# Performance work log

Measured on AMD Instinct MI355X. Metric: run time of the kernel, lower is better.

## Reference

```python
import jax, jax.numpy as jnp
import numpy as np

B, N, F, H, D = 2, 2048, 1024, 16, 64


def setup_inputs() -> dict:
    key = jax.random.key(0)
    ks = jax.random.split(key, 5)
    s = 0.02
    return {
        "x": jax.random.normal(ks[0], (B, N, F), jnp.float32),
        "w_qkv": (jax.random.normal(ks[1], (3 * H * D, F), jnp.float32) * s),
        "w_out": (jax.random.normal(ks[2], (F, H * D), jnp.float32) * s),
        "w_hp_pre": (jax.random.normal(ks[3], (H, H), jnp.float32) * (1.0 / H)),
        "b_hp_pre": jnp.zeros((H,), jnp.float32),
        "w_hp_post": (jax.random.normal(ks[4], (H, H), jnp.float32) * (1.0 / H)),
        "b_hp_post": jnp.zeros((H,), jnp.float32),
    }


def reference(x, w_qkv, w_out, w_hp_pre, b_hp_pre, w_hp_post, b_hp_post):
    b, n, f = x.shape
    # qkv projection; rearrange 'b n (h d qkv) -> qkv b h n d' (qkv innermost)
    proj = (x @ w_qkv.T).reshape(b, n, H, D, 3)
    q = jnp.transpose(proj[..., 0], (0, 2, 1, 3))  # b h n d
    k = jnp.transpose(proj[..., 1], (0, 2, 1, 3))
    v = jnp.transpose(proj[..., 2], (0, 2, 1, 3))
    kv = jnp.stack([k, v], axis=0)  # (2, b, h, n, d) -- returned cache

    scale = D ** -0.5
    dots = jnp.einsum('bhid,bhjd->bhij', q, k) * scale
    # pre talking-heads: 1x1 conv over head channel
    dots = jnp.einsum('gh,bhij->bgij', w_hp_pre, dots) + b_hp_pre[None, :, None, None]
    attn = jax.nn.softmax(dots, axis=-1)
    # post talking-heads
    attn = jnp.einsum('gh,bhij->bgij', w_hp_post, attn) + b_hp_post[None, :, None, None]
    out = jnp.einsum('bhij,bhjd->bhid', attn, v)
    out = jnp.transpose(out, (0, 2, 1, 3)).reshape(b, n, H * D)
    out = out @ w_out.T
    return out, kv
```

## Files before the change

### kernel.cpp

```cpp
#include <hip/hip_runtime.h>
#include <hip/hip_bf16.h>
#include <cstdint>
#include <cstddef>

#define B_ 2
#define N_ 2048
#define F_ 1024
#define H_ 16
#define D_ 64

typedef float f32x4 __attribute__((ext_vector_type(4)));
typedef short s16x8 __attribute__((ext_vector_type(8)));
typedef short s16x4 __attribute__((ext_vector_type(4)));

__device__ __forceinline__ unsigned short f2bf(float f) {
  union { __hip_bfloat16 h; unsigned short u; } c;
  c.h = __float2bfloat16(f);
  return c.u;
}
__device__ __forceinline__ float bf2f(unsigned short u) {
  union { __hip_bfloat16 h; unsigned short u; } c;
  c.u = u;
  return __bfloat162float(c.h);
}

__global__ __launch_bounds__(256) void cvt_bf16(const float* __restrict__ in,
                                                unsigned short* __restrict__ out,
                                                int n8) {
  const int t = blockIdx.x * 256 + threadIdx.x;
  if (t >= n8) return;
  const float4* p = (const float4*)in + (size_t)t * 2;
  float4 a = p[0], b = p[1];
  s16x8 o;
  o[0] = f2bf(a.x); o[1] = f2bf(a.y); o[2] = f2bf(a.z); o[3] = f2bf(a.w);
  o[4] = f2bf(b.x); o[5] = f2bf(b.y); o[6] = f2bf(b.z); o[7] = f2bf(b.w);
  *((s16x8*)out + t) = o;
}

__global__ __launch_bounds__(256) void cvt_wqkv_perm(const float* __restrict__ in,
                                                     unsigned short* __restrict__ out) {
  const int t = blockIdx.x * 256 + threadIdx.x;
  const int rowp = t >> 7;
  const int kk = (t & 127) * 8;
  const int c = rowp >> 10, rem = rowp & 1023;
  const int h = rem >> 6, d = rem & 63;
  const float* p = in + (size_t)(h * 192 + d * 3 + c) * 1024 + kk;
  float4 a = *(const float4*)p, b = *(const float4*)(p + 4);
  s16x8 o;
  o[0] = f2bf(a.x); o[1] = f2bf(a.y); o[2] = f2bf(a.z); o[3] = f2bf(a.w);
  o[4] = f2bf(b.x); o[5] = f2bf(b.y); o[6] = f2bf(b.z); o[7] = f2bf(b.w);
  *((s16x8*)&out[(size_t)rowp * 1024 + kk]) = o;
}

__global__ __launch_bounds__(256) void cvt_sum(const float* __restrict__ a,
                                               const float* __restrict__ b,
                                               unsigned short* __restrict__ out) {
  const int t = blockIdx.x * 256 + threadIdx.x;
  float4 x = *((const float4*)a + t);
  float4 y = *((const float4*)b + t);
  s16x4 o;
  o[0] = f2bf(x.x + y.x); o[1] = f2bf(x.y + y.y);
  o[2] = f2bf(x.z + y.z); o[3] = f2bf(x.w + y.w);
  *((s16x4*)out + t) = o;
}

template <int MODE>
__global__ __launch_bounds__(256) void gemm_bf16(const unsigned short* __restrict__ A,
                                                 const unsigned short* __restrict__ W,
                                                 float* __restrict__ o0,
                                                 unsigned short* __restrict__ oQ,
                                                 unsigned short* __restrict__ oK,
                                                 unsigned short* __restrict__ oVt) {
  __shared__ unsigned short As[128 * 72];
  __shared__ unsigned short Bs[128 * 72];
  const int m0 = blockIdx.y * 128, c0 = blockIdx.x * 128;
  const int tid = threadIdx.x;
  const int wave = tid >> 6, lane = tid & 63;
  const int wm = (wave & 1) * 64, wn = (wave >> 1) * 64;
  const int lm = lane & 15, lq = lane >> 4;
  f32x4 acc[4][4] = {};
  for (int k0 = 0; k0 < 1024; k0 += 64) {
#pragma unroll
    for (int it = 0; it < 4; ++it) {
      const int chunk = it * 256 + tid;
      const int row = chunk >> 3, kq = (chunk & 7) * 8;
      *(float4*)&As[row * 72 + kq] = *(const float4*)&A[(size_t)(m0 + row) * 1024 + k0 + kq];
      *(float4*)&Bs[row * 72 + kq] = *(const float4*)&W[(size_t)(c0 + row) * 1024 + k0 + kq];
    }
    __syncthreads();
#pragma unroll
    for (int ks = 0; ks < 2; ++ks) {
      s16x8 af[4], bfr[4];
#pragma unroll
      for (int i = 0; i < 4; ++i) {
        af[i] = *(const s16x8*)&As[(wm + i * 16 + lm) * 72 + ks * 32 + lq * 8];
        bfr[i] = *(const s16x8*)&Bs[(wn + i * 16 + lm) * 72 + ks * 32 + lq * 8];
      }
#pragma unroll
      for (int i = 0; i < 4; ++i)
#pragma unroll
        for (int j = 0; j < 4; ++j)
          acc[i][j] = __builtin_amdgcn_mfma_f32_16x16x32_bf16(af[i], bfr[j], acc[i][j], 0, 0, 0);
    }
    __syncthreads();
  }
  if (MODE == 1) {
#pragma unroll
    for (int i = 0; i < 4; ++i)
#pragma unroll
      for (int j = 0; j < 4; ++j)
#pragma unroll
        for (int r = 0; r < 4; ++r) {
          const int m = m0 + wm + i * 16 + lq * 4 + r;
          const int col = c0 + wn + j * 16 + lm;
          o0[(size_t)m * 1024 + col] = acc[i][j][r];
        }
  } else {
    const int cls = blockIdx.x >> 3;
    const int colbase = (blockIdx.x & 7) * 128;
    if (cls == 0) {
#pragma unroll
      for (int i = 0; i < 4; ++i)
#pragma unroll
        for (int j = 0; j < 4; ++j) {
          const int cl = colbase + wn + j * 16 + lm;
          const int h = cl >> 6, d = cl & 63;
#pragma unroll
          for (int r = 0; r < 4; ++r) {
            const int m = m0 + wm + i * 16 + lq * 4 + r;
            const int bb = m >> 11, n = m & 2047;
            oQ[(((size_t)bb * H_ + h) * N_ + n) * D_ + d] = f2bf(acc[i][j][r]);
          }
        }
    } else if (cls == 1) {
#pragma unroll
      for (int i = 0; i < 4; ++i)
#pragma unroll
        for (int j = 0; j < 4; ++j) {
          const int cl = colbase + wn + j * 16 + lm;
          const int h = cl >> 6, d = cl & 63;
#pragma unroll
          for (int r = 0; r < 4; ++r) {
            const int m = m0 + wm + i * 16 + lq * 4 + r;
            const int bb = m >> 11, n = m & 2047;
            const size_t idx = (((size_t)bb * H_ + h) * N_ + n) * D_ + d;
            o0[idx] = acc[i][j][r];
            oK[idx] = f2bf(acc[i][j][r]);
          }
        }
    } else {
#pragma unroll
      for (int i = 0; i < 4; ++i) {
        const int n0 = m0 + wm + i * 16 + lq * 4;
        const int bb = n0 >> 11, nl = n0 & 2047;
#pragma unroll
        for (int j = 0; j < 4; ++j) {
          const int cl = colbase + wn + j * 16 + lm;
          const int h = cl >> 6, d = cl & 63;
          s16x4 vp;
#pragma unroll
          for (int r = 0; r < 4; ++r) {
            const size_t idx = (((size_t)bb * H_ + h) * N_ + nl + r) * D_ + d;
            o0[(size_t)B_ * H_ * N_ * D_ + idx] = acc[i][j][r];
            vp[r] = (short)f2bf(acc[i][j][r]);
          }
          *(s16x4*)&oVt[(((size_t)bb * H_ + h) * D_ + d) * N_ + nl] = vp;
        }
      }
    }
  }
}

#define SS_I 648
#define SS_J 20
#define PS_G 1160
#define PS_I 36

__global__ __launch_bounds__(512) void attn_l(const unsigned short* __restrict__ Qb,
                                              const unsigned short* __restrict__ Kb,
                                              const float* __restrict__ wpre,
                                              const float* __restrict__ bpre,
                                              float* __restrict__ l_glob) {
  __shared__ unsigned short Ssh[32 * SS_I];
  const int tid = threadIdx.x;
  const int wave = tid >> 6, lane = tid & 63;
  const int lm = lane & 15, lq = lane >> 4;
  const int b = blockIdx.z, jh = blockIdx.y;
  const int i0 = blockIdx.x * 32;
  const int j00 = jh * 1024;
  const int h0 = wave * 2;

  s16x8 aq[2][2][2];
#pragma unroll
  for (int hh = 0; hh < 2; ++hh)
#pragma unroll
    for (int mi = 0; mi < 2; ++mi)
#pragma unroll
      for (int ks = 0; ks < 2; ++ks)
        aq[hh][mi][ks] = *(const s16x8*)&Qb[(((size_t)(b * H_ + h0 + hh) * N_) + i0 + mi * 16 + lm) * D_ + ks * 32 + lq * 8];

  s16x8 apre;
#pragma unroll
  for (int t = 0; t < 8; ++t) apre[t] = 0;
  if (lq < 2)
#pragma unroll
    for (int t = 0; t < 8; ++t) apre[t] = (short)f2bf(wpre[lm * 16 + lq * 8 + t] * 0.125f);
  float bpre_r[4];
#pragma unroll
  for (int r = 0; r < 4; ++r) bpre_r[r] = bpre[lq * 4 + r];

  float lacc[4][4] = {};

  for (int js = 0; js < 1024; js += 32) {
    const int j0 = j00 + js;
    s16x8 bk[2][2][2];
#pragma unroll
    for (int hh = 0; hh < 2; ++hh)
#pragma unroll
      for (int jt = 0; jt < 2; ++jt)
#pragma unroll
        for (int ks = 0; ks < 2; ++ks)
          bk[hh][jt][ks] = *(const s16x8*)&Kb[(((size_t)(b * H_ + h0 + hh) * N_) + j0 + jt * 16 + lm) * D_ + ks * 32 + lq * 8];
    f32x4 cs[2][2][2];
#pragma unroll
    for (int hh = 0; hh < 2; ++hh)
#pragma unroll
      for (int mi = 0; mi < 2; ++mi)
#pragma unroll
        for (int jt = 0; jt < 2; ++jt) {
          f32x4 c = {};
          c = __builtin_amdgcn_mfma_f32_16x16x32_bf16(aq[hh][mi][0], bk[hh][jt][0], c, 0, 0, 0);
          c = __builtin_amdgcn_mfma_f32_16x16x32_bf16(aq[hh][mi][1], bk[hh][jt][1], c, 0, 0, 0);
          cs[hh][mi][jt] = c;
        }
    __syncthreads();
#pragma unroll
    for (int hh = 0; hh < 2; ++hh)
#pragma unroll
      for (int mi = 0; mi < 2; ++mi)
#pragma unroll
        for (int jt = 0; jt < 2; ++jt)
#pragma unroll
          for (int r = 0; r < 4; ++r)
            Ssh[(mi * 16 + lq * 4 + r) * SS_I + (jt * 16 + lm) * SS_J + h0 + hh] = f2bf(cs[hh][mi][jt][r]);
    __syncthreads();
#pragma unroll
    for (int ii = 0; ii < 4; ++ii) {
      const int i_loc = wave * 4 + ii;
#pragma unroll
      for (int jt = 0; jt < 2; ++jt) {
        s16x8 bs;
#pragma unroll
        for (int t = 0; t < 8; ++t) bs[t] = 0;
        if (lq < 2) {
          s16x4 p0 = *(const s16x4*)&Ssh[i_loc * SS_I + (jt * 16 + lm) * SS_J + lq * 8];
          s16x4 p1 = *(const s16x4*)&Ssh[i_loc * SS_I + (jt * 16 + lm) * SS_J + lq * 8 + 4];
          bs[0] = p0[0]; bs[1] = p0[1]; bs[2] = p0[2]; bs[3] = p0[3];
          bs[4] = p1[0]; bs[5] = p1[1]; bs[6] = p1[2]; bs[7] = p1[3];
        }
        f32x4 c = {};
        c = __builtin_amdgcn_mfma_f32_16x16x32_bf16(apre, bs, c, 0, 0, 0);
#pragma unroll
        for (int r = 0; r < 4; ++r) lacc[ii][r] += __expf(c[r] + bpre_r[r]);
      }
    }
  }
#pragma unroll
  for (int ii = 0; ii < 4; ++ii)
#pragma unroll
    for (int r = 0; r < 4; ++r) {
      float v = lacc[ii][r];
      v += __shfl_xor(v, 1); v += __shfl_xor(v, 2);
      v += __shfl_xor(v, 4); v += __shfl_xor(v, 8);
      if (lm == 0)
        atomicAdd(&l_glob[((size_t)b * N_ + i0 + wave * 4 + ii) * H_ + lq * 4 + r], v);
    }
}

__global__ __launch_bounds__(512) void attn_av(const unsigned short* __restrict__ Qb,
                                               const unsigned short* __restrict__ Kb,
                                               const unsigned short* __restrict__ Vt,
                                               const float* __restrict__ wpre,
                                               const float* __restrict__ bpre,
                                               const float* __restrict__ wpost,
                                               const float* __restrict__ bpost,
                                               const float* __restrict__ l_glob,
                                               float* __restrict__ Opart) {
  __shared__ unsigned short Ssh[32 * SS_I];
  __shared__ unsigned short Esh[32 * SS_I];
  __shared__ unsigned short Psh[16 * PS_G];
  __shared__ float linv[32 * 16];
  const int tid = threadIdx.x;
  const int wave = tid >> 6, lane = tid & 63;
  const int lm = lane & 15, lq = lane >> 4;
  const int b = blockIdx.z, jh = blockIdx.y;
  const int i0 = blockIdx.x * 32;
  const int j00 = jh * 1024;
  const int h0 = wave * 2;
  float* Oout = Opart + (size_t)jh * B_ * N_ * 1024;

  {
    const int il = tid >> 4, g = tid & 15;
    linv[tid] = 1.0f / l_glob[((size_t)b * N_ + i0 + il) * H_ + g];
  }

  s16x8 aq[2][2][2];
#pragma unroll
  for (int hh = 0; hh < 2; ++hh)
#pragma unroll
    for (int mi = 0; mi < 2; ++mi)
#pragma unroll
      for (int ks = 0; ks < 2; ++ks)
        aq[hh][mi][ks] = *(const s16x8*)&Qb[(((size_t)(b * H_ + h0 + hh) * N_) + i0 + mi * 16 + lm) * D_ + ks * 32 + lq * 8];

  s16x8 apre, apost;
#pragma unroll
  for (int t = 0; t < 8; ++t) { apre[t] = 0; apost[t] = 0; }
  if (lq < 2)
#pragma unroll
    for (int t = 0; t < 8; ++t) {
      apre[t] = (short)f2bf(wpre[lm * 16 + lq * 8 + t] * 0.125f);
      apost[t] = (short)f2bf(wpost[lm * 16 + lq * 8 + t]);
    }
  float bpre_r[4], bpost_r[4];
#pragma unroll
  for (int r = 0; r < 4; ++r) {
    bpre_r[r] = bpre[lq * 4 + r];
    bpost_r[r] = bpost[lq * 4 + r];
  }

  f32x4 acc[2][2][4] = {};
  __syncthreads();

  for (int js = 0; js < 1024; js += 32) {
    const int j0 = j00 + js;
    s16x8 bk[2][2][2];
#pragma unroll
    for (int hh = 0; hh < 2; ++hh)
#pragma unroll
      for (int jt = 0; jt < 2; ++jt)
#pragma unroll
        for (int ks = 0; ks < 2; ++ks)
          bk[hh][jt][ks] = *(const s16x8*)&Kb[(((size_t)(b * H_ + h0 + hh) * N_) + j0 + jt * 16 + lm) * D_ + ks * 32 + lq * 8];
    s16x8 bv[2][4];
#pragma unroll
    for (int g = 0; g < 2; ++g)
#pragma unroll
      for (int nd = 0; nd < 4; ++nd)
        bv[g][nd] = *(const s16x8*)&Vt[(((size_t)(b * H_ + h0 + g) * D_) + nd * 16 + lm) * N_ + j0 + lq * 8];

    f32x4 cs[2][2][2];
#pragma unroll
    for (int hh = 0; hh < 2; ++hh)
#pragma unroll
      for (int mi = 0; mi < 2; ++mi)
#pragma unroll
        for (int jt = 0; jt < 2; ++jt) {
          f32x4 c = {};
          c = __builtin_amdgcn_mfma_f32_16x16x32_bf16(aq[hh][mi][0], bk[hh][jt][0], c, 0, 0, 0);
          c = __builtin_amdgcn_mfma_f32_16x16x32_bf16(aq[hh][mi][1], bk[hh][jt][1], c, 0, 0, 0);
          cs[hh][mi][jt] = c;
        }
    __syncthreads();
#pragma unroll
    for (int hh = 0; hh < 2; ++hh)
#pragma unroll
      for (int mi = 0; mi < 2; ++mi)
#pragma unroll
        for (int jt = 0; jt < 2; ++jt)
#pragma unroll
          for (int r = 0; r < 4; ++r)
            Ssh[(mi * 16 + lq * 4 + r) * SS_I + (jt * 16 + lm) * SS_J + h0 + hh] = f2bf(cs[hh][mi][jt][r]);
    __syncthreads();
#pragma unroll
    for (int ii = 0; ii < 4; ++ii) {
      const int i_loc = wave * 4 + ii;
      const float4 li = *(const float4*)&linv[i_loc * 16 + lq * 4];
#pragma unroll
      for (int jt = 0; jt < 2; ++jt) {
        s16x8 bs;
#pragma unroll
        for (int t = 0; t < 8; ++t) bs[t] = 0;
        if (lq < 2) {
          s16x4 p0 = *(const s16x4*)&Ssh[i_loc * SS_I + (jt * 16 + lm) * SS_J + lq * 8];
          s16x4 p1 = *(const s16x4*)&Ssh[i_loc * SS_I + (jt * 16 + lm) * SS_J + lq * 8 + 4];
          bs[0] = p0[0]; bs[1] = p0[1]; bs[2] = p0[2]; bs[3] = p0[3];
          bs[4] = p1[0]; bs[5] = p1[1]; bs[6] = p1[2]; bs[7] = p1[3];
        }
        f32x4 c = {};
        c = __builtin_amdgcn_mfma_f32_16x16x32_bf16(apre, bs, c, 0, 0, 0);
        s16x4 ep;
        const float lif[4] = {li.x, li.y, li.z, li.w};
#pragma unroll
        for (int r = 0; r < 4; ++r)
          ep[r] = (short)f2bf(__expf(c[r] + bpre_r[r]) * lif[r]);
        *(s16x4*)&Esh[i_loc * SS_I + (jt * 16 + lm) * SS_J + lq * 4] = ep;
      }
    }
    __syncthreads();
#pragma unroll
    for (int ii = 0; ii < 4; ++ii) {
      const int i_loc = wave * 4 + ii;
#pragma unroll
      for (int jt = 0; jt < 2; ++jt) {
        s16x8 be;
#pragma unroll
        for (int t = 0; t < 8; ++t) be[t] = 0;
        if (lq < 2) {
          s16x4 p0 = *(const s16x4*)&Esh[i_loc * SS_I + (jt * 16 + lm) * SS_J + lq * 8];
          s16x4 p1 = *(const s16x4*)&Esh[i_loc * SS_I + (jt * 16 + lm) * SS_J + lq * 8 + 4];
          be[0] = p0[0]; be[1] = p0[1]; be[2] = p0[2]; be[3] = p0[3];
          be[4] = p1[0]; be[5] = p1[1]; be[6] = p1[2]; be[7] = p1[3];
        }
        f32x4 c2 = {};
        c2 = __builtin_amdgcn_mfma_f32_16x16x32_bf16(apost, be, c2, 0, 0, 0);
#pragma unroll
        for (int r = 0; r < 4; ++r)
          Psh[(lq * 4 + r) * PS_G + i_loc * PS_I + jt * 16 + lm] = f2bf(c2[r] + bpost_r[r]);
      }
    }
    __syncthreads();
#pragma unroll
    for (int g = 0; g < 2; ++g) {
      const int gg = wave * 2 + g;
#pragma unroll
      for (int mi = 0; mi < 2; ++mi) {
        s16x4 a0 = *(const s16x4*)&Psh[gg * PS_G + (mi * 16 + lm) * PS_I + lq * 8];
        s16x4 a1 = *(const s16x4*)&Psh[gg * PS_G + (mi * 16 + lm) * PS_I + lq * 8 + 4];
        s16x8 ap;
        ap[0] = a0[0]; ap[1] = a0[1]; ap[2] = a0[2]; ap[3] = a0[3];
        ap[4] = a1[0]; ap[5] = a1[1]; ap[6] = a1[2]; ap[7] = a1[3];
#pragma unroll
        for (int nd = 0; nd < 4; ++nd)
          acc[g][mi][nd] = __builtin_amdgcn_mfma_f32_16x16x32_bf16(ap, bv[g][nd], acc[g][mi][nd], 0, 0, 0);
      }
    }
  }
#pragma unroll
  for (int g = 0; g < 2; ++g)
#pragma unroll
    for (int mi = 0; mi < 2; ++mi)
#pragma unroll
      for (int nd = 0; nd < 4; ++nd)
#pragma unroll
        for (int r = 0; r < 4; ++r)
          Oout[((size_t)b * N_ + i0 + mi * 16 + lq * 4 + r) * 1024 + (wave * 2 + g) * 64 + nd * 16 + lm] = acc[g][mi][nd][r];
}

extern "C" void kernel_launch(void* const* d_in, const int* in_sizes, int n_in,
                              void* d_out, int out_size, void* d_ws,
                              size_t ws_size, hipStream_t stream) {
  (void)in_sizes; (void)n_in; (void)out_size; (void)ws_size;
  const float* x      = (const float*)d_in[0];
  const float* w_qkv  = (const float*)d_in[1];
  const float* w_out  = (const float*)d_in[2];
  const float* w_pre  = (const float*)d_in[3];
  const float* b_pre  = (const float*)d_in[4];
  const float* w_post = (const float*)d_in[5];
  const float* b_post = (const float*)d_in[6];

  float* out = (float*)d_out;
  float* kv  = out + (size_t)B_ * N_ * F_;

  unsigned short* xb  = (unsigned short*)d_ws;
  unsigned short* wqb = xb + (size_t)4096 * 1024;
  unsigned short* wob = wqb + (size_t)3072 * 1024;
  unsigned short* Qb  = wob + (size_t)1024 * 1024;
  unsigned short* Kb  = Qb + (size_t)B_ * H_ * N_ * D_;
  unsigned short* Vt  = Kb + (size_t)B_ * H_ * N_ * D_;
  unsigned short* O1  = Vt + (size_t)B_ * H_ * N_ * D_;
  float* l_glob = (float*)(O1 + (size_t)B_ * N_ * F_);
  float* Oh0 = l_glob + (size_t)B_ * N_ * H_;
  float* Oh1 = Oh0 + (size_t)B_ * N_ * F_;

  cvt_bf16<<<dim3(4096 * 1024 / 8 / 256), 256, 0, stream>>>(x, xb, 4096 * 1024 / 8);
  cvt_wqkv_perm<<<dim3(3072 * 128 / 256), 256, 0, stream>>>(w_qkv, wqb);
  cvt_bf16<<<dim3(1024 * 1024 / 8 / 256), 256, 0, stream>>>(w_out, wob, 1024 * 1024 / 8);
  hipMemsetAsync(l_glob, 0, (size_t)B_ * N_ * H_ * 4, stream);

  gemm_bf16<0><<<dim3(3072 / 128, 4096 / 128), 256, 0, stream>>>(xb, wqb, kv, Qb, Kb, Vt);

  attn_l<<<dim3(N_ / 32, 2, B_), 512, 0, stream>>>(Qb, Kb, w_pre, b_pre, l_glob);
  attn_av<<<dim3(N_ / 32, 2, B_), 512, 0, stream>>>(Qb, Kb, Vt, w_pre, b_pre, w_post, b_post,
                                                    l_glob, Oh0);

  cvt_sum<<<dim3(B_ * N_ * F_ / 4 / 256), 256, 0, stream>>>(Oh0, Oh1, O1);

  gemm_bf16<1><<<dim3(1024 / 128, 4096 / 128), 256, 0, stream>>>(O1, wob, out, nullptr, nullptr, nullptr);
}
```

Baseline: 458.5 us.

## Retile attention kernels to 16 query rows and 64-key steps, merging LDS buffers

Both attention kernels now process 16 query rows per block instead of 32, doubling the grid, and step over 64 keys per iteration instead of 32. The S tile is written as packed 32-bit head pairs. In attn_av the separate E buffer is dropped by writing exp values back into the S buffer in place, and the AV product now uses K=64 with two MFMAs per output tile. The intent is to cut LDS footprint and barrier count and raise occupancy and parallelism, at the cost of reloading K/V tiles per 16 rows, which doubles global K/V traffic, and relying on in-place LDS reuse being race-free within a wave.

```diff
diff --git a/kernel.cpp b/kernel.cpp
--- a/kernel.cpp
+++ b/kernel.cpp
@@ -171,33 +171,31 @@
   }
 }
 
-#define SS_I 648
 #define SS_J 20
-#define PS_G 1160
-#define PS_I 36
+#define SS_I 1284
+#define PS_I 68
+#define PS_G 1092
 
 __global__ __launch_bounds__(512) void attn_l(const unsigned short* __restrict__ Qb,
                                               const unsigned short* __restrict__ Kb,
                                               const float* __restrict__ wpre,
                                               const float* __restrict__ bpre,
                                               float* __restrict__ l_glob) {
-  __shared__ unsigned short Ssh[32 * SS_I];
+  __shared__ unsigned short Ssh[16 * SS_I];
   const int tid = threadIdx.x;
   const int wave = tid >> 6, lane = tid & 63;
   const int lm = lane & 15, lq = lane >> 4;
   const int b = blockIdx.z, jh = blockIdx.y;
-  const int i0 = blockIdx.x * 32;
+  const int i0 = blockIdx.x * 16;
   const int j00 = jh * 1024;
   const int h0 = wave * 2;
 
-  s16x8 aq[2][2][2];
+  s16x8 aq[2][2];
 #pragma unroll
   for (int hh = 0; hh < 2; ++hh)
 #pragma unroll
-    for (int mi = 0; mi < 2; ++mi)
-#pragma unroll
-      for (int ks = 0; ks < 2; ++ks)
-        aq[hh][mi][ks] = *(const s16x8*)&Qb[(((size_t)(b * H_ + h0 + hh) * N_) + i0 + mi * 16 + lm) * D_ + ks * 32 + lq * 8];
+    for (int ks = 0; ks < 2; ++ks)
+      aq[hh][ks] = *(const s16x8*)&Qb[(((size_t)(b * H_ + h0 + hh) * N_) + i0 + lm) * D_ + ks * 32 + lq * 8];
 
   s16x8 apre;
 #pragma unroll
@@ -209,71 +207,59 @@
 #pragma unroll
   for (int r = 0; r < 4; ++r) bpre_r[r] = bpre[lq * 4 + r];
 
-  float lacc[4][4] = {};
-
-  for (int js = 0; js < 1024; js += 32) {
+  float lacc[2][4] = {};
+
+  for (int js = 0; js < 1024; js += 64) {
     const int j0 = j00 + js;
-    s16x8 bk[2][2][2];
-#pragma unroll
-    for (int hh = 0; hh < 2; ++hh)
-#pragma unroll
-      for (int jt = 0; jt < 2; ++jt)
-#pragma unroll
-        for (int ks = 0; ks < 2; ++ks)
-          bk[hh][jt][ks] = *(const s16x8*)&Kb[(((size_t)(b * H_ + h0 + hh) * N_) + j0 + jt * 16 + lm) * D_ + ks * 32 + lq * 8];
-    f32x4 cs[2][2][2];
-#pragma unroll
-    for (int hh = 0; hh < 2; ++hh)
-#pragma unroll
-      for (int mi = 0; mi < 2; ++mi)
-#pragma unroll
-        for (int jt = 0; jt < 2; ++jt) {
-          f32x4 c = {};
-          c = __builtin_amdgcn_mfma_f32_16x16x32_bf16(aq[hh][mi][0], bk[hh][jt][0], c, 0, 0, 0);
-          c = __builtin_amdgcn_mfma_f32_16x16x32_bf16(aq[hh][mi][1], bk[hh][jt][1], c, 0, 0, 0);
-          cs[hh][mi][jt] = c;
-        }
-    __syncthreads();
-#pragma unroll
-    for (int hh = 0; hh < 2; ++hh)
-#pragma unroll
-      for (int mi = 0; mi < 2; ++mi)
-#pragma unroll
-        for (int jt = 0; jt < 2; ++jt)
-#pragma unroll
-          for (int r = 0; r < 4; ++r)
-            Ssh[(mi * 16 + lq * 4 + r) * SS_I + (jt * 16 + lm) * SS_J + h0 + hh] = f2bf(cs[hh][mi][jt][r]);
-    __syncthreads();
-#pragma unroll
-    for (int ii = 0; ii < 4; ++ii) {
-      const int i_loc = wave * 4 + ii;
-#pragma unroll
-      for (int jt = 0; jt < 2; ++jt) {
-        s16x8 bs;
-#pragma unroll
-        for (int t = 0; t < 8; ++t) bs[t] = 0;
-        if (lq < 2) {
-          s16x4 p0 = *(const s16x4*)&Ssh[i_loc * SS_I + (jt * 16 + lm) * SS_J + lq * 8];
-          s16x4 p1 = *(const s16x4*)&Ssh[i_loc * SS_I + (jt * 16 + lm) * SS_J + lq * 8 + 4];
-          bs[0] = p0[0]; bs[1] = p0[1]; bs[2] = p0[2]; bs[3] = p0[3];
-          bs[4] = p1[0]; bs[5] = p1[1]; bs[6] = p1[2]; bs[7] = p1[3];
-        }
-        f32x4 c = {};
-        c = __builtin_amdgcn_mfma_f32_16x16x32_bf16(apre, bs, c, 0, 0, 0);
-#pragma unroll
-        for (int r = 0; r < 4; ++r) lacc[ii][r] += __expf(c[r] + bpre_r[r]);
-      }
+    __syncthreads();
+#pragma unroll
+    for (int jt = 0; jt < 4; ++jt) {
+      f32x4 c[2];
+#pragma unroll
+      for (int hh = 0; hh < 2; ++hh) {
+        const unsigned short* kp = &Kb[(((size_t)(b * H_ + h0 + hh) * N_) + j0 + jt * 16 + lm) * D_ + lq * 8];
+        s16x8 b0 = *(const s16x8*)kp;
+        s16x8 b1 = *(const s16x8*)(kp + 32);
+        f32x4 cc = {};
+        cc = __builtin_amdgcn_mfma_f32_16x16x32_bf16(aq[hh][0], b0, cc, 0, 0, 0);
+        cc = __builtin_amdgcn_mfma_f32_16x16x32_bf16(aq[hh][1], b1, cc, 0, 0, 0);
+        c[hh] = cc;
+      }
+#pragma unroll
+      for (int r = 0; r < 4; ++r) {
+        unsigned int pk = (unsigned int)f2bf(c[0][r]) | ((unsigned int)f2bf(c[1][r]) << 16);
+        *(unsigned int*)&Ssh[(lq * 4 + r) * SS_I + (jt * 16 + lm) * SS_J + h0] = pk;
+      }
+    }
+    __syncthreads();
+#pragma unroll
+    for (int ii = 0; ii < 8; ++ii) {
+      const int ig = ii >> 2, jt = ii & 3;
+      const int i_loc = wave * 2 + ig;
+      s16x8 bs;
+#pragma unroll
+      for (int t = 0; t < 8; ++t) bs[t] = 0;
+      if (lq < 2) {
+        s16x4 p0 = *(const s16x4*)&Ssh[i_loc * SS_I + (jt * 16 + lm) * SS_J + lq * 8];
+        s16x4 p1 = *(const s16x4*)&Ssh[i_loc * SS_I + (jt * 16 + lm) * SS_J + lq * 8 + 4];
+        bs[0] = p0[0]; bs[1] = p0[1]; bs[2] = p0[2]; bs[3] = p0[3];
+        bs[4] = p1[0]; bs[5] = p1[1]; bs[6] = p1[2]; bs[7] = p1[3];
+      }
+      f32x4 c = {};
+      c = __builtin_amdgcn_mfma_f32_16x16x32_bf16(apre, bs, c, 0, 0, 0);
+#pragma unroll
+      for (int r = 0; r < 4; ++r) lacc[ig][r] += __expf(c[r] + bpre_r[r]);
     }
   }
 #pragma unroll
-  for (int ii = 0; ii < 4; ++ii)
+  for (int ig = 0; ig < 2; ++ig)
 #pragma unroll
     for (int r = 0; r < 4; ++r) {
-      float v = lacc[ii][r];
+      float v = lacc[ig][r];
       v += __shfl_xor(v, 1); v += __shfl_xor(v, 2);
       v += __shfl_xor(v, 4); v += __shfl_xor(v, 8);
       if (lm == 0)
-        atomicAdd(&l_glob[((size_t)b * N_ + i0 + wave * 4 + ii) * H_ + lq * 4 + r], v);
+        atomicAdd(&l_glob[((size_t)b * N_ + i0 + wave * 2 + ig) * H_ + lq * 4 + r], v);
     }
 }
 
@@ -286,32 +272,27 @@
                                                const float* __restrict__ bpost,
                                                const float* __restrict__ l_glob,
                                                float* __restrict__ Opart) {
-  __shared__ unsigned short Ssh[32 * SS_I];
-  __shared__ unsigned short Esh[32 * SS_I];
+  __shared__ unsigned short Ssh[16 * SS_I];
   __shared__ unsigned short Psh[16 * PS_G];
-  __shared__ float linv[32 * 16];
+  __shared__ float linv[256];
   const int tid = threadIdx.x;
   const int wave = tid >> 6, lane = tid & 63;
   const int lm = lane & 15, lq = lane >> 4;
   const int b = blockIdx.z, jh = blockIdx.y;
-  const int i0 = blockIdx.x * 32;
+  const int i0 = blockIdx.x * 16;
   const int j00 = jh * 1024;
   const int h0 = wave * 2;
-  float* Oout = Opart + (size_t)jh * B_ * N_ * 1024;
-
-  {
-    const int il = tid >> 4, g = tid & 15;
-    linv[tid] = 1.0f / l_glob[((size_t)b * N_ + i0 + il) * H_ + g];
-  }
-
-  s16x8 aq[2][2][2];
+  float* Oout = Opart + (size_t)jh * ((size_t)B_ * N_ * 1024);
+
+  if (tid < 256)
+    linv[tid] = 1.0f / l_glob[((size_t)b * N_ + i0 + (tid >> 4)) * H_ + (tid & 15)];
+
+  s16x8 aq[2][2];
 #pragma unroll
   for (int hh = 0; hh < 2; ++hh)
 #pragma unroll
-    for (int mi = 0; mi < 2; ++mi)
-#pragma unroll
-      for (int ks = 0; ks < 2; ++ks)
-        aq[hh][mi][ks] = *(const s16x8*)&Qb[(((size_t)(b * H_ + h0 + hh) * N_) + i0 + mi * 16 + lm) * D_ + ks * 32 + lq * 8];
+    for (int ks = 0; ks < 2; ++ks)
+      aq[hh][ks] = *(const s16x8*)&Qb[(((size_t)(b * H_ + h0 + hh) * N_) + i0 + lm) * D_ + ks * 32 + lq * 8];
 
   s16x8 apre, apost;
 #pragma unroll
@@ -329,122 +310,97 @@
     bpost_r[r] = bpost[lq * 4 + r];
   }
 
-  f32x4 acc[2][2][4] = {};
-  __syncthreads();
-
-  for (int js = 0; js < 1024; js += 32) {
+  f32x4 acc[2][4] = {};
+
+  for (int js = 0; js < 1024; js += 64) {
     const int j0 = j00 + js;
-    s16x8 bk[2][2][2];
-#pragma unroll
-    for (int hh = 0; hh < 2; ++hh)
-#pragma unroll
-      for (int jt = 0; jt < 2; ++jt)
-#pragma unroll
-        for (int ks = 0; ks < 2; ++ks)
-          bk[hh][jt][ks] = *(const s16x8*)&Kb[(((size_t)(b * H_ + h0 + hh) * N_) + j0 + jt * 16 + lm) * D_ + ks * 32 + lq * 8];
-    s16x8 bv[2][4];
-#pragma unroll
-    for (int g = 0; g < 2; ++g)
-#pragma unroll
-      for (int nd = 0; nd < 4; ++nd)
-        bv[g][nd] = *(const s16x8*)&Vt[(((size_t)(b * H_ + h0 + g) * D_) + nd * 16 + lm) * N_ + j0 + lq * 8];
-
-    f32x4 cs[2][2][2];
-#pragma unroll
-    for (int hh = 0; hh < 2; ++hh)
-#pragma unroll
-      for (int mi = 0; mi < 2; ++mi)
-#pragma unroll
-        for (int jt = 0; jt < 2; ++jt) {
-          f32x4 c = {};
-          c = __builtin_amdgcn_mfma_f32_16x16x32_bf16(aq[hh][mi][0], bk[hh][jt][0], c, 0, 0, 0);
-          c = __builtin_amdgcn_mfma_f32_16x16x32_bf16(aq[hh][mi][1], bk[hh][jt][1], c, 0, 0, 0);
-          cs[hh][mi][jt] = c;
-        }
-    __syncthreads();
-#pragma unroll
-    for (int hh = 0; hh < 2; ++hh)
-#pragma unroll
-      for (int mi = 0; mi < 2; ++mi)
-#pragma unroll
-        for (int jt = 0; jt < 2; ++jt)
-#pragma unroll
-          for (int r = 0; r < 4; ++r)
-            Ssh[(mi * 16 + lq * 4 + r) * SS_I + (jt * 16 + lm) * SS_J + h0 + hh] = f2bf(cs[hh][mi][jt][r]);
-    __syncthreads();
-#pragma unroll
-    for (int ii = 0; ii < 4; ++ii) {
-      const int i_loc = wave * 4 + ii;
+#pragma unroll
+    for (int jt = 0; jt < 4; ++jt) {
+      f32x4 c[2];
+#pragma unroll
+      for (int hh = 0; hh < 2; ++hh) {
+        const unsigned short* kp = &Kb[(((size_t)(b * H_ + h0 + hh) * N_) + j0 + jt * 16 + lm) * D_ + lq * 8];
+        s16x8 b0 = *(const s16x8*)kp;
+        s16x8 b1 = *(const s16x8*)(kp + 32);
+        f32x4 cc = {};
+        cc = __builtin_amdgcn_mfma_f32_16x16x32_bf16(aq[hh][0], b0, cc, 0, 0, 0);
+        cc = __builtin_amdgcn_mfma_f32_16x16x32_bf16(aq[hh][1], b1, cc, 0, 0, 0);
+        c[hh] = cc;
+      }
+#pragma unroll
+      for (int r = 0; r < 4; ++r) {
+        unsigned int pk = (unsigned int)f2bf(c[0][r]) | ((unsigned int)f2bf(c[1][r]) << 16);
+        *(unsigned int*)&Ssh[(lq * 4 + r) * SS_I + (jt * 16 + lm) * SS_J + h0] = pk;
+      }
+    }
+    __syncthreads();
+#pragma unroll
+    for (int ii = 0; ii < 8; ++ii) {
+      const int ig = ii >> 2, jt = ii & 3;
+      const int i_loc = wave * 2 + ig;
+      const unsigned short* srow = &Ssh[i_loc * SS_I + (jt * 16 + lm) * SS_J];
+      s16x8 bs;
+#pragma unroll
+      for (int t = 0; t < 8; ++t) bs[t] = 0;
+      if (lq < 2) {
+        s16x4 p0 = *(const s16x4*)(srow + lq * 8);
+        s16x4 p1 = *(const s16x4*)(srow + lq * 8 + 4);
+        bs[0] = p0[0]; bs[1] = p0[1]; bs[2] = p0[2]; bs[3] = p0[3];
+        bs[4] = p1[0]; bs[5] = p1[1]; bs[6] = p1[2]; bs[7] = p1[3];
+      }
+      f32x4 c = {};
+      c = __builtin_amdgcn_mfma_f32_16x16x32_bf16(apre, bs, c, 0, 0, 0);
       const float4 li = *(const float4*)&linv[i_loc * 16 + lq * 4];
-#pragma unroll
-      for (int jt = 0; jt < 2; ++jt) {
-        s16x8 bs;
-#pragma unroll
-        for (int t = 0; t < 8; ++t) bs[t] = 0;
-        if (lq < 2) {
-          s16x4 p0 = *(const s16x4*)&Ssh[i_loc * SS_I + (jt * 16 + lm) * SS_J + lq * 8];
-          s16x4 p1 = *(const s16x4*)&Ssh[i_loc * SS_I + (jt * 16 + lm) * SS_J + lq * 8 + 4];
-          bs[0] = p0[0]; bs[1] = p0[1]; bs[2] = p0[2]; bs[3] = p0[3];
-          bs[4] = p1[0]; bs[5] = p1[1]; bs[6] = p1[2]; bs[7] = p1[3];
-        }
-        f32x4 c = {};
-        c = __builtin_amdgcn_mfma_f32_16x16x32_bf16(apre, bs, c, 0, 0, 0);
-        s16x4 ep;
-        const float lif[4] = {li.x, li.y, li.z, li.w};
-#pragma unroll
-        for (int r = 0; r < 4; ++r)
-          ep[r] = (short)f2bf(__expf(c[r] + bpre_r[r]) * lif[r]);
-        *(s16x4*)&Esh[i_loc * SS_I + (jt * 16 + lm) * SS_J + lq * 4] = ep;
-      }
-    }
-    __syncthreads();
-#pragma unroll
-    for (int ii = 0; ii < 4; ++ii) {
-      const int i_loc = wave * 4 + ii;
-#pragma unroll
-      for (int jt = 0; jt < 2; ++jt) {
-        s16x8 be;
-#pragma unroll
-        for (int t = 0; t < 8; ++t) be[t] = 0;
-        if (lq < 2) {
-          s16x4 p0 = *(const s16x4*)&Esh[i_loc * SS_I + (jt * 16 + lm) * SS_J + lq * 8];
-          s16x4 p1 = *(const s16x4*)&Esh[i_loc * SS_I + (jt * 16 + lm) * SS_J + lq * 8 + 4];
-          be[0] = p0[0]; be[1] = p0[1]; be[2] = p0[2]; be[3] = p0[3];
-          be[4] = p1[0]; be[5] = p1[1]; be[6] = p1[2]; be[7] = p1[3];
-        }
-        f32x4 c2 = {};
-        c2 = __builtin_amdgcn_mfma_f32_16x16x32_bf16(apost, be, c2, 0, 0, 0);
-#pragma unroll
-        for (int r = 0; r < 4; ++r)
-          Psh[(lq * 4 + r) * PS_G + i_loc * PS_I + jt * 16 + lm] = f2bf(c2[r] + bpost_r[r]);
-      }
+      const float lif[4] = {li.x, li.y, li.z, li.w};
+      s16x4 ep;
+#pragma unroll
+      for (int r = 0; r < 4; ++r)
+        ep[r] = (short)f2bf(__expf(c[r] + bpre_r[r]) * lif[r]);
+      *(s16x4*)&Ssh[i_loc * SS_I + (jt * 16 + lm) * SS_J + lq * 4] = ep;
+      s16x8 be;
+#pragma unroll
+      for (int t = 0; t < 8; ++t) be[t] = 0;
+      if (lq < 2) {
+        s16x4 q0 = *(const s16x4*)(srow + lq * 8);
+        s16x4 q1 = *(const s16x4*)(srow + lq * 8 + 4);
+        be[0] = q0[0]; be[1] = q0[1]; be[2] = q0[2]; be[3] = q0[3];
+        be[4] = q1[0]; be[5] = q1[1]; be[6] = q1[2]; be[7] = q1[3];
+      }
+      f32x4 c2 = {};
+      c2 = __builtin_amdgcn_mfma_f32_16x16x32_bf16(apost, be, c2, 0, 0, 0);
+#pragma unroll
+      for (int r = 0; r < 4; ++r)
+        Psh[(lq * 4 + r) * PS_G + i_loc * PS_I + jt * 16 + lm] = f2bf(c2[r] + bpost_r[r]);
     }
     __syncthreads();
 #pragma unroll
     for (int g = 0; g < 2; ++g) {
-      const int gg = wave * 2 + g;
-#pragma unroll
-      for (int mi = 0; mi < 2; ++mi) {
-        s16x4 a0 = *(const s16x4*)&Psh[gg * PS_G + (mi * 16 + lm) * PS_I + lq * 8];
-        s16x4 a1 = *(const s16x4*)&Psh[gg * PS_G + (mi * 16 + lm) * PS_I + lq * 8 + 4];
-        s16x8 ap;
-        ap[0] = a0[0]; ap[1] = a0[1]; ap[2] = a0[2]; ap[3] = a0[3];
-        ap[4] = a1[0]; ap[5] = a1[1]; ap[6] = a1[2]; ap[7] = a1[3];
-#pragma unroll
-        for (int nd = 0; nd < 4; ++nd)
-          acc[g][mi][nd] = __builtin_amdgcn_mfma_f32_16x16x32_bf16(ap, bv[g][nd], acc[g][mi][nd], 0, 0, 0);
+      const int gg = h0 + g;
+      s16x8 ap[2];
+#pragma unroll
+      for (int ks = 0; ks < 2; ++ks) {
+        s16x4 a0 = *(const s16x4*)&Psh[gg * PS_G + lm * PS_I + ks * 32 + lq * 8];
+        s16x4 a1 = *(const s16x4*)&Psh[gg * PS_G + lm * PS_I + ks * 32 + lq * 8 + 4];
+        ap[ks][0] = a0[0]; ap[ks][1] = a0[1]; ap[ks][2] = a0[2]; ap[ks][3] = a0[3];
+        ap[ks][4] = a1[0]; ap[ks][5] = a1[1]; ap[ks][6] = a1[2]; ap[ks][7] = a1[3];
+      }
+#pragma unroll
+      for (int nd = 0; nd < 4; ++nd) {
+        const unsigned short* vp = &Vt[(((size_t)(b * H_ + gg) * D_) + nd * 16 + lm) * N_ + j0 + lq * 8];
+        s16x8 v0 = *(const s16x8*)vp;
+        s16x8 v1 = *(const s16x8*)(vp + 32);
+        acc[g][nd] = __builtin_amdgcn_mfma_f32_16x16x32_bf16(ap[0], v0, acc[g][nd], 0, 0, 0);
+        acc[g][nd] = __builtin_amdgcn_mfma_f32_16x16x32_bf16(ap[1], v1, acc[g][nd], 0, 0, 0);
       }
     }
   }
 #pragma unroll
   for (int g = 0; g < 2; ++g)
 #pragma unroll
-    for (int mi = 0; mi < 2; ++mi)
-#pragma unroll
-      for (int nd = 0; nd < 4; ++nd)
-#pragma unroll
-        for (int r = 0; r < 4; ++r)
-          Oout[((size_t)b * N_ + i0 + mi * 16 + lq * 4 + r) * 1024 + (wave * 2 + g) * 64 + nd * 16 + lm] = acc[g][mi][nd][r];
+    for (int nd = 0; nd < 4; ++nd)
+#pragma unroll
+      for (int r = 0; r < 4; ++r)
+        Oout[((size_t)b * N_ + i0 + lq * 4 + r) * 1024 + (h0 + g) * 64 + nd * 16 + lm] = acc[g][nd][r];
 }
 
 extern "C" void kernel_launch(void* const* d_in, const int* in_sizes, int n_in,
@@ -480,8 +436,8 @@
 
   gemm_bf16<0><<<dim3(3072 / 128, 4096 / 128), 256, 0, stream>>>(xb, wqb, kv, Qb, Kb, Vt);
 
-  attn_l<<<dim3(N_ / 32, 2, B_), 512, 0, stream>>>(Qb, Kb, w_pre, b_pre, l_glob);
-  attn_av<<<dim3(N_ / 32, 2, B_), 512, 0, stream>>>(Qb, Kb, Vt, w_pre, b_pre, w_post, b_post,
+  attn_l<<<dim3(N_ / 16, 2, B_), 512, 0, stream>>>(Qb, Kb, w_pre, b_pre, l_glob);
+  attn_av<<<dim3(N_ / 16, 2, B_), 512, 0, stream>>>(Qb, Kb, Vt, w_pre, b_pre, w_post, b_post,
                                                     l_glob, Oh0);
 
   cvt_sum<<<dim3(B_ * N_ * F_ / 4 / 256), 256, 0, stream>>>(Oh0, Oh1, O1);
```

Measured after the change: 604.4 us. +31.8%, slower.
